# Kernel tuning notes

Hardware: AMD Instinct MI355X
Metric: run time of the kernel (lower is better)

Reference implementation:

```python
import jax, jax.numpy as jnp
import numpy as np

B, C, Hf, T = 8, 2, 257, 2048
D_IN = C * Hf          # 514
DM = 256               # d_model
NL = 4                 # n_layers
N = 32                 # S4D complex state size (d_state=64 -> N=32 complex modes)


def setup_inputs() -> dict:
    key = jax.random.key(0)
    ks = jax.random.split(key, 16)
    sc_in = 1.0 / np.sqrt(D_IN)
    sc_dm = 1.0 / np.sqrt(DM)
    inp = {}
    inp['x'] = jax.random.normal(ks[0], (B, C, Hf, T, 2), dtype=jnp.float32)
    # complex encoder (d_input -> d_model)
    inp['enc_Wr'] = jax.random.normal(ks[1], (DM, D_IN), dtype=jnp.float32) * sc_in
    inp['enc_Wi'] = jax.random.normal(ks[2], (DM, D_IN), dtype=jnp.float32) * sc_in
    inp['enc_br'] = jnp.zeros((DM,), jnp.float32)
    inp['enc_bi'] = jnp.zeros((DM,), jnp.float32)
    # per-layer S4D kernel params (stacked over layers)
    lo, hi = np.log(0.001), np.log(0.1)
    inp['log_dt'] = jax.random.uniform(ks[3], (NL, DM), dtype=jnp.float32) * (hi - lo) + lo
    inp['log_A_real'] = jnp.full((NL, DM, N), np.log(0.5), dtype=jnp.float32)
    inp['A_imag'] = jnp.broadcast_to(np.pi * jnp.arange(N, dtype=jnp.float32), (NL, DM, N)) + 0.0
    inp['C_r'] = jax.random.normal(ks[4], (NL, DM, N), dtype=jnp.float32)
    inp['C_i'] = jax.random.normal(ks[5], (NL, DM, N), dtype=jnp.float32)
    inp['D'] = jax.random.normal(ks[6], (NL, DM), dtype=jnp.float32)
    # per-layer complex pointwise output linear (d_model -> d_model)
    inp['out_Wr'] = jax.random.normal(ks[7], (NL, DM, DM), dtype=jnp.float32) * sc_dm
    inp['out_Wi'] = jax.random.normal(ks[8], (NL, DM, DM), dtype=jnp.float32) * sc_dm
    inp['out_br'] = jnp.zeros((NL, DM), jnp.float32)
    inp['out_bi'] = jnp.zeros((NL, DM), jnp.float32)
    # per-layer complex LayerNorm (separate real/imag affine)
    inp['ln_gamma_r'] = jnp.ones((NL, DM), jnp.float32)
    inp['ln_gamma_i'] = jnp.ones((NL, DM), jnp.float32)
    inp['ln_beta_r'] = jnp.zeros((NL, DM), jnp.float32)
    inp['ln_beta_i'] = jnp.zeros((NL, DM), jnp.float32)
    # complex decoder (d_model -> d_output = c*h)
    inp['dec_Wr'] = jax.random.normal(ks[9], (D_IN, DM), dtype=jnp.float32) * sc_dm
    inp['dec_Wi'] = jax.random.normal(ks[10], (D_IN, DM), dtype=jnp.float32) * sc_dm
    inp['dec_br'] = jnp.zeros((D_IN,), jnp.float32)
    inp['dec_bi'] = jnp.zeros((D_IN,), jnp.float32)
    return inp


def _clinear(xr, xi, Wr, Wi, br, bi):
    # complex linear: (xr + i xi) @ (Wr + i Wi)^T + (br + i bi)
    yr = xr @ Wr.T - xi @ Wi.T + br
    yi = xi @ Wr.T + xr @ Wi.T + bi
    return yr, yi


def _layernorm_ch(v, g, b, eps=1e-5):
    # normalize over channel axis 1 of (B, H, T)
    m = v.mean(axis=1, keepdims=True)
    var = ((v - m) ** 2).mean(axis=1, keepdims=True)
    return (v - m) / jnp.sqrt(var + eps) * g[None, :, None] + b[None, :, None]


def _forward(x, enc_Wr, enc_Wi, enc_br, enc_bi, log_dt, log_A_real, A_imag,
             C_r, C_i, D, out_Wr, out_Wi, out_br, out_bi,
             ln_gamma_r, ln_gamma_i, ln_beta_r, ln_beta_i,
             dec_Wr, dec_Wi, dec_br, dec_bi):
    b, c, h, T, _ = x.shape
    xf = x.reshape(b, c * h, T, 2)
    xf = jnp.swapaxes(xf, 1, 2)               # (b, T, c*h, 2)
    zr, zi = _clinear(xf[..., 0], xf[..., 1], enc_Wr, enc_Wi, enc_br, enc_bi)  # (b, T, DM)
    zr = jnp.swapaxes(zr, -1, -2)             # (b, DM, T)
    zi = jnp.swapaxes(zi, -1, -2)
    tgrid = jnp.arange(T, dtype=jnp.float32)
    n_layers = log_dt.shape[0]
    for l in range(n_layers):
        # ---- ComplexS4D kernel (diagonal SSM, ZOH-like discretization) ----
        dt = jnp.exp(log_dt[l])[:, None]                        # (H,1)
        A = -jnp.exp(log_A_real[l]) + 1j * A_imag[l]            # (H,N) complex
        dtA = A * dt                                            # (H,N)
        Ct = (C_r[l] + 1j * C_i[l]) * (jnp.exp(dtA) - 1.0) / A  # (H,N)
        K = jnp.einsum('hn,hnl->hl', Ct, jnp.exp(dtA[:, :, None] * tgrid))  # complex (H,T)
        # ---- complex FFT causal convolution ----
        u = zr + 1j * zi                                        # (b,H,T)
        y = jnp.fft.ifft(jnp.fft.fft(u, 2 * T) * jnp.fft.fft(K, 2 * T)[None])[..., :T]
        y = y + D[l][None, :, None] * u                         # skip connection
        yr = jax.nn.gelu(y.real)
        yi = jax.nn.gelu(y.imag)
        # ---- complex pointwise output linear ----
        orr = jnp.einsum('bht,gh->bgt', yr, out_Wr[l]) - jnp.einsum('bht,gh->bgt', yi, out_Wi[l]) + out_br[l][None, :, None]
        oii = jnp.einsum('bht,gh->bgt', yi, out_Wr[l]) + jnp.einsum('bht,gh->bgt', yr, out_Wi[l]) + out_bi[l][None, :, None]
        # residual + post-norm (prenorm=False), complex LayerNorm over d_model
        zr = _layernorm_ch(zr + orr, ln_gamma_r[l], ln_beta_r[l])
        zi = _layernorm_ch(zi + oii, ln_gamma_i[l], ln_beta_i[l])
    zr = jnp.swapaxes(zr, -1, -2)             # (b, T, DM)
    zi = jnp.swapaxes(zi, -1, -2)
    dr, di = _clinear(zr, zi, dec_Wr, dec_Wi, dec_br, dec_bi)  # (b, T, c*h)
    dr = jnp.swapaxes(dr, 1, 2)               # (b, c*h, T)
    di = jnp.swapaxes(di, 1, 2)
    return jnp.stack([dr, di], axis=-1).reshape(b, c, h, T, 2)


def reference(x, enc_Wr, enc_Wi, enc_br, enc_bi, log_dt, log_A_real, A_imag,
              C_r, C_i, D, out_Wr, out_Wi, out_br, out_bi,
              ln_gamma_r, ln_gamma_i, ln_beta_r, ln_beta_i,
              dec_Wr, dec_Wi, dec_br, dec_bi):
    return _forward(x, enc_Wr, enc_Wi, enc_br, enc_bi, log_dt, log_A_real, A_imag,
                    C_r, C_i, D, out_Wr, out_Wi, out_br, out_bi,
                    ln_gamma_r, ln_gamma_i, ln_beta_r, ln_beta_i,
                    dec_Wr, dec_Wi, dec_br, dec_bi)
```

## Files before the change

### kernel.cpp

```cpp
#include <hip/hip_runtime.h>
#include <cstddef>
#include <cstdint>


typedef __attribute__((ext_vector_type(8))) short short8;
typedef __attribute__((ext_vector_type(4))) float float4v;

__device__ __forceinline__ unsigned short f2bf(float f) {
    union { float f; unsigned u; } v; v.f = f;
    const unsigned r = v.u + 0x7fffu + ((v.u >> 16) & 1u);
    return (unsigned short)(r >> 16);
}

__device__ __forceinline__ float gelu_tanh(float x) {
    const float x3 = x * x * x;
    const float v  = 0.7978845608028654f * (x + 0.044715f * x3);
    const float e  = __expf(2.f * v);
    const float th = 1.f - 2.f / (e + 1.f);
    return 0.5f * x * (1.f + th);
}

template<int CTL>
__device__ __forceinline__ float dppadd(float x) {
    union { float f; int i; } a, r;
    a.f = x;
    r.i = __builtin_amdgcn_update_dpp(a.i, a.i, CTL, 0xF, 0xF, true);
    return x + r.f;
}
#define DPP_XOR1 0xB1
#define DPP_XOR2 0x4E

#define ASYNC_COPY16(gp, lp) __builtin_amdgcn_global_load_lds( \
    (const __attribute__((address_space(1))) unsigned int*)(gp), \
    (__attribute__((address_space(3))) unsigned int*)(lp), 16, 0, 0)

__global__ __launch_bounds__(256) void buildw_k(
    const float* __restrict__ Wr, const float* __restrict__ Wi,
    unsigned short* __restrict__ A, int G, int H, int Hoff, int Kp, int Mp)
{
    const long long i = (long long)blockIdx.x * 256 + threadIdx.x;
    if (i >= (long long)Mp * Kp) return;
    const int m = (int)(i / Kp), k = (int)(i % Kp);
    float val = 0.f;
    if (m < 2 * G) {
        const int ri = m >= G;
        const int g = m - ri * G;
        const int blk = k >= Hoff;
        const int hh = k - blk * Hoff;
        if (hh < H) {
            const float wr = Wr[(size_t)g * H + hh];
            const float wi = Wi[(size_t)g * H + hh];
            val = ri ? (blk ? wr : wi) : (blk ? -wi : wr);
        }
    }
    A[i] = f2bf(val);
}

__global__ __launch_bounds__(256) void buildwL_k(
    const float* __restrict__ Wr0, const float* __restrict__ Wi0,
    unsigned short* __restrict__ A0)
{
    const int l = blockIdx.y;
    const float* Wr = Wr0 + (size_t)l * 65536;
    const float* Wi = Wi0 + (size_t)l * 65536;
    unsigned short* A = A0 + (size_t)l * 262144;
    const int i = blockIdx.x * 256 + threadIdx.x;
    const int m = i >> 9, k = i & 511;
    const int ri = m >= 256;
    const int g = m & 255;
    const int blk = k >> 8;
    const int hh = k & 255;
    const float wr = Wr[(size_t)g * 256 + hh];
    const float wi = Wi[(size_t)g * 256 + hh];
    const float val = ri ? (blk ? wr : wi) : (blk ? -wi : wr);
    A[i] = f2bf(val);
}

__global__ __launch_bounds__(256) void build_bias_k(
    const float* __restrict__ br, const float* __restrict__ bi,
    float* __restrict__ bias, int G)
{
    const int i = blockIdx.x * 256 + threadIdx.x;
    if (i < G) bias[i] = br[i];
    else if (i < 2 * G) bias[i] = bi[i - G];
}

__global__ __launch_bounds__(256) void build_biasL_k(
    const float* __restrict__ br0, const float* __restrict__ bi0,
    float* __restrict__ bias0)
{
    const int l = blockIdx.y;
    const int i = blockIdx.x * 256 + threadIdx.x;
    const float* br = br0 + l * 256;
    const float* bi = bi0 + l * 256;
    float* bias = bias0 + l * 512;
    if (i < 256) bias[i] = br[i];
    else bias[i] = bi[i - 256];
}

__global__ __launch_bounds__(256) void packx_k(const float* __restrict__ x,
                                               unsigned short* __restrict__ xp)
{
    const int t0 = blockIdx.x * 64, d0 = blockIdx.y * 64, b = blockIdx.z;
    __shared__ unsigned short tr_[64][72];
    __shared__ unsigned short ti_[64][72];
    const int tid = threadIdx.x;
    const int tp = tid & 31, dl0 = tid >> 5;
#pragma unroll
    for (int p = 0; p < 8; ++p) {
        const int d = dl0 + p * 8;
        const int gd = d0 + d;
        float4 v = make_float4(0.f, 0.f, 0.f, 0.f);
        if (gd < 514) v = *(const float4*)(x + (((size_t)b * 514 + gd) * 2048 + t0 + tp * 2) * 2);
        tr_[tp * 2 + 0][d] = f2bf(v.x); ti_[tp * 2 + 0][d] = f2bf(v.y);
        tr_[tp * 2 + 1][d] = f2bf(v.z); ti_[tp * 2 + 1][d] = f2bf(v.w);
    }
    __syncthreads();
    const int dc = tid & 7;
    const int kloc = d0 + dc * 8;
    if (kloc < 528) {
#pragma unroll
        for (int p = 0; p < 2; ++p) {
            const int t = (tid >> 3) + p * 32;
            const size_t rowb = ((size_t)b * 2048 + t0 + t) * 1056;
            *(short8*)&xp[rowb + kloc]       = *(const short8*)&tr_[t][dc * 8];
            *(short8*)&xp[rowb + 528 + kloc] = *(const short8*)&ti_[t][dc * 8];
        }
    }
}

__global__ __launch_bounds__(256) void trz_k(const float* __restrict__ sf,
                                             unsigned short* __restrict__ dst)
{
    const int t0 = blockIdx.x * 64, k0 = blockIdx.y * 64, b = blockIdx.z;
    __shared__ unsigned short tile[64][72];
    const int tid = threadIdx.x;
    const int tp = tid & 31, kl0 = tid >> 5;
#pragma unroll
    for (int p = 0; p < 8; ++p) {
        const int kl = kl0 + p * 8;
        const float2 v = *(const float2*)(sf + ((size_t)b * 512 + k0 + kl) * 2048 + t0 + tp * 2);
        tile[tp * 2 + 0][kl] = f2bf(v.x);
        tile[tp * 2 + 1][kl] = f2bf(v.y);
    }
    __syncthreads();
    const int dc = tid & 7;
#pragma unroll
    for (int p = 0; p < 2; ++p) {
        const int t = (tid >> 3) + p * 32;
        *(short8*)&dst[((size_t)b * 2048 + t0 + t) * 512 + k0 + dc * 8] = *(const short8*)&tile[t][dc * 8];
    }
}

template<int MODE>
__global__ __launch_bounds__(256, 2) void mgemm_k(
    const unsigned short* __restrict__ A, const float* __restrict__ bias,
    const unsigned short* __restrict__ Bm, float* __restrict__ out,
    int M, int Kp)
{
    __shared__ unsigned short As[4096];
    __shared__ unsigned short Bs[4096];
    const int tid = threadIdx.x;
    const int w = tid >> 6, lane = tid & 63;
    const int m0 = blockIdx.x * 128, t0 = blockIdx.y * 128, b = blockIdx.z;
    const int wm = w & 1, wn = w >> 1;

    const unsigned short* Ab = A + (size_t)m0 * Kp;
    const unsigned short* Bb = Bm + ((size_t)b * 2048 + t0) * Kp;

    const int c0 = w * 64 + lane;
    const int r0 = c0 >> 2, q0 = (c0 & 3) * 8;
    const int c1 = c0 + 256;
    const int r1 = c1 >> 2, q1 = (c1 & 3) * 8;
    unsigned short* As0 = &As[(size_t)(w * 64) * 8];
    unsigned short* As1 = &As[(size_t)(w * 64 + 256) * 8];
    unsigned short* Bs0 = &Bs[(size_t)(w * 64) * 8];
    unsigned short* Bs1 = &Bs[(size_t)(w * 64 + 256) * 8];

    float4v acc[4][4];
#pragma unroll
    for (int i = 0; i < 4; ++i)
#pragma unroll
        for (int j = 0; j < 4; ++j) acc[i][j] = (float4v){0.f, 0.f, 0.f, 0.f};

    const int arow = wm * 64 + (lane & 15);
    const int brow = wn * 64 + (lane & 15);
    const int kq = (lane >> 4) * 8;

    for (int k0 = 0; k0 < Kp; k0 += 32) {
        ASYNC_COPY16(Ab + (size_t)r0 * Kp + k0 + q0, As0);
        ASYNC_COPY16(Ab + (size_t)r1 * Kp + k0 + q1, As1);
        ASYNC_COPY16(Bb + (size_t)r0 * Kp + k0 + q0, Bs0);
        ASYNC_COPY16(Bb + (size_t)r1 * Kp + k0 + q1, Bs1);
        __syncthreads();
        short8 af[4], bf[4];
#pragma unroll
        for (int i = 0; i < 4; ++i) af[i] = *(const short8*)&As[(arow + i * 16) * 32 + kq];
#pragma unroll
        for (int j = 0; j < 4; ++j) bf[j] = *(const short8*)&Bs[(brow + j * 16) * 32 + kq];
#pragma unroll
        for (int i = 0; i < 4; ++i)
#pragma unroll
            for (int j = 0; j < 4; ++j)
                acc[i][j] = __builtin_amdgcn_mfma_f32_16x16x32_bf16(af[i], bf[j], acc[i][j], 0, 0, 0);
        __syncthreads();
    }

    const int col = lane & 15;
    const int rq = (lane >> 4) * 4;
#pragma unroll
    for (int i = 0; i < 4; ++i) {
        const int mloc = wm * 64 + i * 16 + rq;
#pragma unroll
        for (int r = 0; r < 4; ++r) {
            const int m = m0 + mloc + r;
            if (MODE == 1 && m >= M) continue;
            const float bs = bias[m];
#pragma unroll
            for (int j = 0; j < 4; ++j) {
                const int t = t0 + wn * 64 + j * 16 + col;
                const float vv = acc[i][j][r] + bs;
                if (MODE == 0) {
                    out[((size_t)b * 512 + m) * 2048 + t] = vv;
                } else {
                    const int comp = m >= 514;
                    const int g = m - 514 * comp;
                    out[(((size_t)b * 514 + g) * 2048 + t) * 2 + comp] = vv;
                }
            }
        }
    }
}

__global__ __launch_bounds__(512, 2) void mgemmln_k(
    const unsigned short* __restrict__ A, const float* __restrict__ bias,
    const unsigned short* __restrict__ Bm, float* __restrict__ z,
    const float* __restrict__ gamr, const float* __restrict__ gami,
    const float* __restrict__ betr, const float* __restrict__ beti, int l)
{
    __shared__ unsigned short Bs[64][512];
    __shared__ float biasS[512], gamS[512], betS[512];
    __shared__ float sred[8][64][2];
    __shared__ float sstat[2][64][2];
    const int tid = threadIdx.x;
    const int w = tid >> 6, lane = tid & 63;
    const int t0g = blockIdx.x * 64, b = blockIdx.y;
    unsigned char* BsB = (unsigned char*)&Bs[0][0];

    {
        const unsigned short* ysrc = Bm + (size_t)b * 512 * 2048 + t0g;
        const int tseg = lane & 7;
        const int rloc = lane >> 3;
#pragma unroll
        for (int p = 0; p < 8; ++p) {
            const int krow = w * 8 + rloc + p * 64;
            const short8 v = *(const short8*)(ysrc + (size_t)krow * 2048 + tseg * 8);
#pragma unroll
            for (int j = 0; j < 8; ++j) {
                const int t = tseg * 8 + j;
                const int mask = (((t & 7) ^ ((t >> 3) & 7)) << 4);
                *(unsigned short*)(BsB + t * 1024 + ((krow * 2) ^ mask)) =
                    ((const unsigned short*)&v)[j];
            }
        }
        const int m = tid, g = m & 255, comp = m >> 8;
        biasS[m] = bias[m];
        gamS[m] = (comp ? gami : gamr)[l * 256 + g];
        betS[m] = (comp ? beti : betr)[l * 256 + g];
    }
    __syncthreads();

    float4v acc[4][4];
#pragma unroll
    for (int i = 0; i < 4; ++i)
#pragma unroll
        for (int j = 0; j < 4; ++j) acc[i][j] = (float4v){0.f, 0.f, 0.f, 0.f};

    const int brow = lane & 15;
    const int kq8 = (lane >> 4) * 8;
    const unsigned short* Ab = A + ((size_t)(w * 64 + brow)) * 512 + kq8;
    int baseB[4], maskB[4];
#pragma unroll
    for (int j = 0; j < 4; ++j) {
        const int t = j * 16 + brow;
        baseB[j] = t * 1024;
        maskB[j] = (((t & 7) ^ ((t >> 3) & 7)) << 4);
    }

#define LOADF(af_, bf_, k0_) do {                                              \
    _Pragma("unroll")                                                          \
    for (int i = 0; i < 4; ++i)                                                \
        af_[i] = *(const short8*)(Ab + (size_t)i * 16 * 512 + (k0_));          \
    _Pragma("unroll")                                                          \
    for (int j = 0; j < 4; ++j)                                                \
        bf_[j] = *(const short8*)(BsB + baseB[j] + ((((k0_) + kq8) * 2) ^ maskB[j])); \
} while (0)
#define MFMAS(af_, bf_) do {                                                   \
    _Pragma("unroll")                                                          \
    for (int i = 0; i < 4; ++i)                                                \
        _Pragma("unroll")                                                      \
        for (int j = 0; j < 4; ++j)                                            \
            acc[i][j] = __builtin_amdgcn_mfma_f32_16x16x32_bf16(af_[i], bf_[j], acc[i][j], 0, 0, 0); \
} while (0)

    {
        short8 afA[4], bfA[4], afB[4], bfB[4];
        LOADF(afA, bfA, 0);
#pragma unroll 1
        for (int kk = 0; kk < 16; kk += 2) {
            LOADF(afB, bfB, kk * 32 + 32);
            MFMAS(afA, bfA);
            if (kk + 2 < 16) LOADF(afA, bfA, kk * 32 + 64);
            MFMAS(afB, bfB);
        }
    }
#undef LOADF
#undef MFMAS

    const int q4 = (lane >> 4) * 4;
    float4 b4[4], g4[4], e4[4];
#pragma unroll
    for (int i = 0; i < 4; ++i) {
        const int m0 = w * 64 + i * 16 + q4;
        b4[i] = *(const float4*)&biasS[m0];
        g4[i] = *(const float4*)&gamS[m0];
        e4[i] = *(const float4*)&betS[m0];
    }

    float s1[4], s2[4];
#pragma unroll
    for (int j = 0; j < 4; ++j) { s1[j] = 0.f; s2[j] = 0.f; }
#pragma unroll
    for (int j = 0; j < 4; ++j) {
        const int t = t0g + j * 16 + brow;
#pragma unroll
        for (int i = 0; i < 4; ++i) {
            const int m = w * 64 + i * 16 + q4;
            const float* zp = &z[((size_t)b * 512 + m) * 2048 + t];
            const float bb[4] = {b4[i].x, b4[i].y, b4[i].z, b4[i].w};
#pragma unroll
            for (int r = 0; r < 4; ++r) {
                const float v = acc[i][j][r] + bb[r] + zp[(size_t)r * 2048];
                acc[i][j][r] = v;
                s1[j] += v; s2[j] += v * v;
            }
        }
    }
#pragma unroll
    for (int j = 0; j < 4; ++j) {
        s1[j] += __shfl_xor(s1[j], 16); s2[j] += __shfl_xor(s2[j], 16);
        s1[j] += __shfl_xor(s1[j], 32); s2[j] += __shfl_xor(s2[j], 32);
    }
    if (lane < 16) {
#pragma unroll
        for (int j = 0; j < 4; ++j) {
            sred[w][j * 16 + lane][0] = s1[j];
            sred[w][j * 16 + lane][1] = s2[j];
        }
    }
    __syncthreads();
    if (tid < 128) {
        const int t = tid & 63, comp = tid >> 6;
        float S1 = 0.f, S2 = 0.f;
#pragma unroll
        for (int w2 = 0; w2 < 4; ++w2) {
            S1 += sred[comp * 4 + w2][t][0];
            S2 += sred[comp * 4 + w2][t][1];
        }
        const float mn = S1 * (1.f / 256.f);
        const float var = S2 * (1.f / 256.f) - mn * mn;
        sstat[comp][t][0] = mn;
        sstat[comp][t][1] = rsqrtf(var + 1e-5f);
    }
    __syncthreads();
    const int comp = w >> 2;
#pragma unroll
    for (int j = 0; j < 4; ++j) {
        const int tl = j * 16 + brow;
        const float mn = sstat[comp][tl][0], rs = sstat[comp][tl][1];
        const int t = t0g + tl;
#pragma unroll
        for (int i = 0; i < 4; ++i) {
            const int m = w * 64 + i * 16 + q4;
            float* zp = &z[((size_t)b * 512 + m) * 2048 + t];
            const float gg[4] = {g4[i].x, g4[i].y, g4[i].z, g4[i].w};
            const float ee[4] = {e4[i].x, e4[i].y, e4[i].z, e4[i].w};
#pragma unroll
            for (int r = 0; r < 4; ++r)
                zp[(size_t)r * 2048] = (acc[i][j][r] - mn) * rs * gg[r] + ee[r];
        }
    }
}

__global__ __launch_bounds__(256, 4) void s4scan_k(
    const float* __restrict__ z, unsigned short* __restrict__ y,
    const float* __restrict__ log_dt, const float* __restrict__ log_A_real,
    const float* __restrict__ A_imag, const float* __restrict__ C_r,
    const float* __restrict__ C_i, const float* __restrict__ Dsk, int l)
{
    const int h = blockIdx.x, b = blockIdx.y;
    const int tid = threadIdx.x;
    const int lane = tid & 63, wv = tid >> 6;
    __shared__ float2 wsh[32], csh[32];
    __shared__ float dsh;
    __shared__ float2 us[64][33];
    __shared__ __align__(16) unsigned char uni[64 * 33 * 8];
    float2 (*vsh2)[33] = (float2(*)[33])uni;
    float2 (*ys)[33]   = (float2(*)[33])uni;

    if (tid < 32) {
        const size_t pidx = ((size_t)l * 256 + h) * 32 + tid;
        const float dt = __expf(log_dt[l * 256 + h]);
        const float Ar = -__expf(log_A_real[pidx]);
        const float Ai = A_imag[pidx];
        const float er = __expf(Ar * dt);
        float sv, cv;
        __sincosf(Ai * dt, &sv, &cv);
        const float wr = er * cv, wi = er * sv;
        const float den = 1.f / (Ar * Ar + Ai * Ai);
        const float nr = wr - 1.f, ni = wi;
        const float qr = (nr * Ar + ni * Ai) * den;
        const float qi = (ni * Ar - nr * Ai) * den;
        const float cr = C_r[pidx], ci = C_i[pidx];
        wsh[tid] = make_float2(wr, wi);
        csh[tid] = make_float2(cr * qr - ci * qi, cr * qi + ci * qr);
    }
    if (tid == 32) dsh = Dsk[l * 256 + h];

    const int c0q = tid >> 2, t0q = (tid & 3) * 8;
    {
        const float* zrp = z + ((size_t)b * 512 + h) * 2048 + tid * 8;
        const float* zip = zrp + 256 * 2048;
        const float4 r0 = *(const float4*)zrp, r1 = *(const float4*)(zrp + 4);
        const float4 i0 = *(const float4*)zip, i1 = *(const float4*)(zip + 4);
        float2* up = &us[c0q][t0q];
        up[0] = make_float2(r0.x, i0.x); up[1] = make_float2(r0.y, i0.y);
        up[2] = make_float2(r0.z, i0.z); up[3] = make_float2(r0.w, i0.w);
        up[4] = make_float2(r1.x, i1.x); up[5] = make_float2(r1.y, i1.y);
        up[6] = make_float2(r1.z, i1.z); up[7] = make_float2(r1.w, i1.w);
    }
    __syncthreads();

    {
        float2 w8[8], x8[8];
#pragma unroll
        for (int j = 0; j < 8; ++j) {
            w8[j] = wsh[wv * 8 + j];
            x8[j] = make_float2(0.f, 0.f);
        }
#pragma unroll 8
        for (int tt = 0; tt < 32; ++tt) {
            const float2 u = us[lane][tt];
#pragma unroll
            for (int j = 0; j < 8; ++j) {
                const float nxr = __builtin_fmaf(w8[j].x, x8[j].x, __builtin_fmaf(-w8[j].y, x8[j].y, u.x));
                const float nxi = __builtin_fmaf(w8[j].x, x8[j].y, __builtin_fmaf(w8[j].y, x8[j].x, u.y));
                x8[j].x = nxr; x8[j].y = nxi;
            }
        }
#pragma unroll
        for (int j = 0; j < 8; ++j) {
            float fr = w8[j].x, fi = w8[j].y;
#pragma unroll
            for (int s = 0; s < 5; ++s) { const float a2 = fr * fr - fi * fi, b2 = 2.f * fr * fi; fr = a2; fi = b2; }
            float qrv = x8[j].x, qiv = x8[j].y, pr = fr, pi = fi;
#pragma unroll
            for (int s = 0; s < 6; ++s) {
                const int d = 1 << s;
                const float sr = __shfl_up(qrv, (unsigned)d);
                const float si = __shfl_up(qiv, (unsigned)d);
                if (lane >= d) {
                    qrv += pr * sr - pi * si;
                    qiv += pr * si + pi * sr;
                }
                const float a2 = pr * pr - pi * pi, b2 = 2.f * pr * pi;
                pr = a2; pi = b2;
            }
            float vr = __shfl_up(qrv, 1u);
            float vi = __shfl_up(qiv, 1u);
            if (lane == 0) { vr = 0.f; vi = 0.f; }
            vsh2[lane][wv * 8 + j] = make_float2(vr, vi);
        }
    }
    __syncthreads();

    {
        const int q = tid & 3;
        float2 w8[8], c8[8], s8[8];
#pragma unroll
        for (int j = 0; j < 8; ++j) {
            const int n = q * 8 + j;
            w8[j] = wsh[n];
            c8[j] = csh[n];
            s8[j] = vsh2[c0q][n];
        }
        __syncthreads();
#pragma unroll 4
        for (int tt = 0; tt < 32; ++tt) {
            const float2 u = us[c0q][tt];
            float pyr = 0.f, pyi = 0.f;
#pragma unroll
            for (int j = 0; j < 8; ++j) {
                const float nsr = __builtin_fmaf(w8[j].x, s8[j].x, __builtin_fmaf(-w8[j].y, s8[j].y, u.x));
                const float nsi = __builtin_fmaf(w8[j].x, s8[j].y, __builtin_fmaf(w8[j].y, s8[j].x, u.y));
                s8[j].x = nsr; s8[j].y = nsi;
                pyr = __builtin_fmaf(c8[j].x, nsr, __builtin_fmaf(-c8[j].y, nsi, pyr));
                pyi = __builtin_fmaf(c8[j].x, nsi, __builtin_fmaf(c8[j].y, nsr, pyi));
            }
            pyr = dppadd<DPP_XOR1>(pyr); pyr = dppadd<DPP_XOR2>(pyr);
            pyi = dppadd<DPP_XOR1>(pyi); pyi = dppadd<DPP_XOR2>(pyi);
            if (q == 0) ys[c0q][tt] = make_float2(pyr, pyi);
        }
    }
    __syncthreads();

    {
        const float dv = dsh;
        unsigned short* yrp = y + ((size_t)b * 512 + h) * 2048 + tid * 8;
        unsigned short* yip = yrp + 256 * 2048;
        short8 vr8, vi8;
#pragma unroll
        for (int j = 0; j < 8; ++j) {
            const float2 yv = ys[c0q][t0q + j];
            const float2 uv = us[c0q][t0q + j];
            ((unsigned short*)&vr8)[j] = f2bf(gelu_tanh(__builtin_fmaf(dv, uv.x, yv.x)));
            ((unsigned short*)&vi8)[j] = f2bf(gelu_tanh(__builtin_fmaf(dv, uv.y, yv.y)));
        }
        *(short8*)yrp = vr8;
        *(short8*)yip = vi8;
    }
}

extern "C" void kernel_launch(void* const* d_in, const int* in_sizes, int n_in,
                              void* d_out, int out_size, void* d_ws, size_t ws_size,
                              hipStream_t stream)
{
    const float* x        = (const float*)d_in[0];
    const float* enc_Wr   = (const float*)d_in[1];
    const float* enc_Wi   = (const float*)d_in[2];
    const float* enc_br   = (const float*)d_in[3];
    const float* enc_bi   = (const float*)d_in[4];
    const float* log_dt   = (const float*)d_in[5];
    const float* log_A_r  = (const float*)d_in[6];
    const float* A_imag   = (const float*)d_in[7];
    const float* C_r      = (const float*)d_in[8];
    const float* C_i      = (const float*)d_in[9];
    const float* Dp       = (const float*)d_in[10];
    const float* out_Wr   = (const float*)d_in[11];
    const float* out_Wi   = (const float*)d_in[12];
    const float* out_br   = (const float*)d_in[13];
    const float* out_bi   = (const float*)d_in[14];
    const float* ln_gr    = (const float*)d_in[15];
    const float* ln_gi    = (const float*)d_in[16];
    const float* ln_br    = (const float*)d_in[17];
    const float* ln_bi    = (const float*)d_in[18];
    const float* dec_Wr   = (const float*)d_in[19];
    const float* dec_Wi   = (const float*)d_in[20];
    const float* dec_br   = (const float*)d_in[21];
    const float* dec_bi   = (const float*)d_in[22];

    uint8_t* W = (uint8_t*)d_ws;
    float* z             = (float*)W;
    unsigned short* zp   = (unsigned short*)(W + 33554432);
    unsigned short* A_enc= (unsigned short*)(W + 50331648);
    unsigned short* A_lay= (unsigned short*)(W + 51412992);
    unsigned short* A_dec= (unsigned short*)(W + 53510144);
    float* b_enc         = (float*)(W + 54689792);
    float* b_lay         = (float*)(W + 54691840);
    float* b_dec         = (float*)(W + 54700032);

    unsigned short* y   = (unsigned short*)((uint8_t*)d_out + 33554432);
    unsigned short* xp  = (unsigned short*)d_out;

    buildw_k<<<2112, 256, 0, stream>>>(enc_Wr, enc_Wi, A_enc, 256, 514, 528, 1056, 512);
    buildwL_k<<<dim3(1024, 4), 256, 0, stream>>>(out_Wr, out_Wi, A_lay);
    buildw_k<<<2304, 256, 0, stream>>>(dec_Wr, dec_Wi, A_dec, 514, 256, 256, 512, 1152);
    build_bias_k<<<2, 256, 0, stream>>>(enc_br, enc_bi, b_enc, 256);
    build_biasL_k<<<dim3(2, 4), 256, 0, stream>>>(out_br, out_bi, b_lay);
    build_bias_k<<<5, 256, 0, stream>>>(dec_br, dec_bi, b_dec, 514);

    packx_k<<<dim3(32, 9, 8), 256, 0, stream>>>(x, xp);
    mgemm_k<0><<<dim3(4, 16, 8), 256, 0, stream>>>(A_enc, b_enc, xp, z, 512, 1056);

    for (int l = 0; l < 4; ++l) {
        s4scan_k<<<dim3(256, 8), 256, 0, stream>>>(z, y, log_dt, log_A_r, A_imag, C_r, C_i, Dp, l);
        mgemmln_k<<<dim3(32, 8), 512, 0, stream>>>(A_lay + (size_t)l * 262144,
                                                   b_lay + l * 512, y, z,
                                                   ln_gr, ln_gi, ln_br, ln_bi, l);
    }

    trz_k<<<dim3(32, 8, 8), 256, 0, stream>>>(z, zp);
    mgemm_k<1><<<dim3(9, 16, 8), 256, 0, stream>>>(A_dec, b_dec, zp, (float*)d_out, 1028, 512);
}
```

Measured before the change: 593.3 us.

## Fuse decoder transpose into GEMM, merge weight-build kernels, trim scan shuffle

The separate z-transpose/bf16-pack kernel and the decoder GEMM are replaced by one decoder kernel. It loads fp32 z directly, converts it to bf16 into a swizzled LDS tile covering the full K=512, and streams A fragments from global memory with double-buffered registers. The six weight and bias preparation launches are merged into a single kernel. The scan replaces a shuffle-up with a shifted LDS store. The aim is to cut launch overhead and the zp round trip through memory, at the cost of redundant z reads across the three M-blocks and uncached global A loads.

```diff
diff --git a/kernel.cpp b/kernel.cpp
--- a/kernel.cpp
+++ b/kernel.cpp
@@ -34,68 +34,85 @@
     (const __attribute__((address_space(1))) unsigned int*)(gp), \
     (__attribute__((address_space(3))) unsigned int*)(lp), 16, 0, 0)
 
-__global__ __launch_bounds__(256) void buildw_k(
-    const float* __restrict__ Wr, const float* __restrict__ Wi,
-    unsigned short* __restrict__ A, int G, int H, int Hoff, int Kp, int Mp)
+__global__ __launch_bounds__(256) void buildall_k(
+    const float* __restrict__ enc_Wr, const float* __restrict__ enc_Wi,
+    const float* __restrict__ out_Wr, const float* __restrict__ out_Wi,
+    const float* __restrict__ dec_Wr, const float* __restrict__ dec_Wi,
+    const float* __restrict__ enc_br, const float* __restrict__ enc_bi,
+    const float* __restrict__ out_br, const float* __restrict__ out_bi,
+    const float* __restrict__ dec_br, const float* __restrict__ dec_bi,
+    unsigned short* __restrict__ A_enc, unsigned short* __restrict__ A_lay,
+    unsigned short* __restrict__ A_dec,
+    float* __restrict__ b_enc, float* __restrict__ b_lay,
+    float* __restrict__ b_dec)
 {
-    const long long i = (long long)blockIdx.x * 256 + threadIdx.x;
-    if (i >= (long long)Mp * Kp) return;
-    const int m = (int)(i / Kp), k = (int)(i % Kp);
-    float val = 0.f;
-    if (m < 2 * G) {
-        const int ri = m >= G;
-        const int g = m - ri * G;
-        const int blk = k >= Hoff;
-        const int hh = k - blk * Hoff;
-        if (hh < H) {
-            const float wr = Wr[(size_t)g * H + hh];
-            const float wi = Wi[(size_t)g * H + hh];
-            val = ri ? (blk ? wr : wi) : (blk ? -wi : wr);
-        }
-    }
-    A[i] = f2bf(val);
-}
-
-__global__ __launch_bounds__(256) void buildwL_k(
-    const float* __restrict__ Wr0, const float* __restrict__ Wi0,
-    unsigned short* __restrict__ A0)
-{
-    const int l = blockIdx.y;
-    const float* Wr = Wr0 + (size_t)l * 65536;
-    const float* Wi = Wi0 + (size_t)l * 65536;
-    unsigned short* A = A0 + (size_t)l * 262144;
-    const int i = blockIdx.x * 256 + threadIdx.x;
-    const int m = i >> 9, k = i & 511;
-    const int ri = m >= 256;
-    const int g = m & 255;
-    const int blk = k >> 8;
-    const int hh = k & 255;
-    const float wr = Wr[(size_t)g * 256 + hh];
-    const float wi = Wi[(size_t)g * 256 + hh];
-    const float val = ri ? (blk ? wr : wi) : (blk ? -wi : wr);
-    A[i] = f2bf(val);
-}
-
-__global__ __launch_bounds__(256) void build_bias_k(
-    const float* __restrict__ br, const float* __restrict__ bi,
-    float* __restrict__ bias, int G)
-{
-    const int i = blockIdx.x * 256 + threadIdx.x;
-    if (i < G) bias[i] = br[i];
-    else if (i < 2 * G) bias[i] = bi[i - G];
-}
-
-__global__ __launch_bounds__(256) void build_biasL_k(
-    const float* __restrict__ br0, const float* __restrict__ bi0,
-    float* __restrict__ bias0)
-{
-    const int l = blockIdx.y;
-    const int i = blockIdx.x * 256 + threadIdx.x;
-    const float* br = br0 + l * 256;
-    const float* bi = bi0 + l * 256;
-    float* bias = bias0 + l * 512;
-    if (i < 256) bias[i] = br[i];
-    else bias[i] = bi[i - 256];
+    int blk = blockIdx.x;
+    const int tid = threadIdx.x;
+    if (blk < 2112) {
+        const int i = blk * 256 + tid;
+        const int m = i / 1056, k = i - m * 1056;
+        const int ri = m >= 256, g = m & 255;
+        const int blk2 = k >= 528;
+        const int hh = k - blk2 * 528;
+        float val = 0.f;
+        if (hh < 514) {
+            const float wr = enc_Wr[(size_t)g * 514 + hh];
+            const float wi = enc_Wi[(size_t)g * 514 + hh];
+            val = ri ? (blk2 ? wr : wi) : (blk2 ? -wi : wr);
+        }
+        A_enc[i] = f2bf(val);
+        return;
+    }
+    blk -= 2112;
+    if (blk < 4096) {
+        const int l = blk >> 10;
+        const int i = ((blk & 1023) << 8) + tid;
+        const float* Wr = out_Wr + (size_t)l * 65536;
+        const float* Wi = out_Wi + (size_t)l * 65536;
+        const int m = i >> 9, k = i & 511;
+        const int ri = m >= 256, g = m & 255;
+        const int blk2 = k >> 8, hh = k & 255;
+        const float wr = Wr[(size_t)g * 256 + hh];
+        const float wi = Wi[(size_t)g * 256 + hh];
+        A_lay[(size_t)l * 262144 + i] =
+            f2bf(ri ? (blk2 ? wr : wi) : (blk2 ? -wi : wr));
+        return;
+    }
+    blk -= 4096;
+    if (blk < 2304) {
+        const int i = blk * 256 + tid;
+        const int m = i >> 9, k = i & 511;
+        float val = 0.f;
+        if (m < 1028) {
+            const int ri = m >= 514;
+            const int g = m - 514 * ri;
+            const int blk2 = k >> 8, hh = k & 255;
+            const float wr = dec_Wr[(size_t)g * 256 + hh];
+            const float wi = dec_Wi[(size_t)g * 256 + hh];
+            val = ri ? (blk2 ? wr : wi) : (blk2 ? -wi : wr);
+        }
+        A_dec[i] = f2bf(val);
+        return;
+    }
+    blk -= 2304;
+    if (blk < 2) {
+        const int i = blk * 256 + tid;
+        b_enc[i] = (i < 256) ? enc_br[i] : enc_bi[i - 256];
+        return;
+    }
+    blk -= 2;
+    if (blk < 8) {
+        const int l = blk >> 1;
+        const int i = ((blk & 1) << 8) + tid;
+        b_lay[l * 512 + i] = (i < 256) ? out_br[l * 256 + i]
+                                       : out_bi[l * 256 + i - 256];
+        return;
+    }
+    blk -= 8;
+    {
+        const int i = blk * 256 + tid;
+        if (i < 1028) b_dec[i] = (i < 514) ? dec_br[i] : dec_bi[i - 514];
+    }
 }
 
 __global__ __launch_bounds__(256) void packx_k(const float* __restrict__ x,
@@ -129,30 +146,6 @@
     }
 }
 
-__global__ __launch_bounds__(256) void trz_k(const float* __restrict__ sf,
-                                             unsigned short* __restrict__ dst)
-{
-    const int t0 = blockIdx.x * 64, k0 = blockIdx.y * 64, b = blockIdx.z;
-    __shared__ unsigned short tile[64][72];
-    const int tid = threadIdx.x;
-    const int tp = tid & 31, kl0 = tid >> 5;
-#pragma unroll
-    for (int p = 0; p < 8; ++p) {
-        const int kl = kl0 + p * 8;
-        const float2 v = *(const float2*)(sf + ((size_t)b * 512 + k0 + kl) * 2048 + t0 + tp * 2);
-        tile[tp * 2 + 0][kl] = f2bf(v.x);
-        tile[tp * 2 + 1][kl] = f2bf(v.y);
-    }
-    __syncthreads();
-    const int dc = tid & 7;
-#pragma unroll
-    for (int p = 0; p < 2; ++p) {
-        const int t = (tid >> 3) + p * 32;
-        *(short8*)&dst[((size_t)b * 2048 + t0 + t) * 512 + k0 + dc * 8] = *(const short8*)&tile[t][dc * 8];
-    }
-}
-
-template<int MODE>
 __global__ __launch_bounds__(256, 2) void mgemm_k(
     const unsigned short* __restrict__ A, const float* __restrict__ bias,
     const unsigned short* __restrict__ Bm, float* __restrict__ out,
@@ -214,19 +207,11 @@
 #pragma unroll
         for (int r = 0; r < 4; ++r) {
             const int m = m0 + mloc + r;
-            if (MODE == 1 && m >= M) continue;
             const float bs = bias[m];
 #pragma unroll
             for (int j = 0; j < 4; ++j) {
                 const int t = t0 + wn * 64 + j * 16 + col;
-                const float vv = acc[i][j][r] + bs;
-                if (MODE == 0) {
-                    out[((size_t)b * 512 + m) * 2048 + t] = vv;
-                } else {
-                    const int comp = m >= 514;
-                    const int g = m - 514 * comp;
-                    out[(((size_t)b * 514 + g) * 2048 + t) * 2 + comp] = vv;
-                }
+                out[((size_t)b * 512 + m) * 2048 + t] = acc[i][j][r] + bs;
             }
         }
     }
@@ -388,6 +373,103 @@
 #pragma unroll
             for (int r = 0; r < 4; ++r)
                 zp[(size_t)r * 2048] = (acc[i][j][r] - mn) * rs * gg[r] + ee[r];
+        }
+    }
+}
+
+__global__ __launch_bounds__(512, 2) void mgemmdec_k(
+    const unsigned short* __restrict__ A, const float* __restrict__ bias,
+    const float* __restrict__ z, float* __restrict__ out)
+{
+    __shared__ unsigned short Bs[64][512];
+    const int tid = threadIdx.x;
+    const int w = tid >> 6, lane = tid & 63;
+    const int m0b = blockIdx.x * 384;
+    const int t0g = blockIdx.y * 64, b = blockIdx.z;
+    unsigned char* BsB = (unsigned char*)&Bs[0][0];
+
+    {
+        const float* zsrc = z + (size_t)b * 512 * 2048 + t0g;
+        const int tseg = lane & 7, rloc = lane >> 3;
+#pragma unroll
+        for (int p = 0; p < 8; ++p) {
+            const int krow = w * 8 + rloc + p * 64;
+            const float* rowp = zsrc + (size_t)krow * 2048 + tseg * 8;
+            const float4 va = *(const float4*)rowp;
+            const float4 vb = *(const float4*)(rowp + 4);
+            const float vals[8] = {va.x, va.y, va.z, va.w, vb.x, vb.y, vb.z, vb.w};
+#pragma unroll
+            for (int j = 0; j < 8; ++j) {
+                const int t = tseg * 8 + j;
+                const int mask = (((t & 7) ^ ((t >> 3) & 7)) << 4);
+                *(unsigned short*)(BsB + t * 1024 + ((krow * 2) ^ mask)) = f2bf(vals[j]);
+            }
+        }
+    }
+    __syncthreads();
+
+    float4v acc[3][4];
+#pragma unroll
+    for (int i = 0; i < 3; ++i)
+#pragma unroll
+        for (int j = 0; j < 4; ++j) acc[i][j] = (float4v){0.f, 0.f, 0.f, 0.f};
+
+    const int brow = lane & 15;
+    const int kq8 = (lane >> 4) * 8;
+    const unsigned short* Ab = A + ((size_t)(m0b + w * 48 + brow)) * 512 + kq8;
+    int baseB[4], maskB[4];
+#pragma unroll
+    for (int j = 0; j < 4; ++j) {
+        const int t = j * 16 + brow;
+        baseB[j] = t * 1024;
+        maskB[j] = (((t & 7) ^ ((t >> 3) & 7)) << 4);
+    }
+
+#define LOADF(af_, bf_, k0_) do {                                              \
+    _Pragma("unroll")                                                          \
+    for (int i = 0; i < 3; ++i)                                                \
+        af_[i] = *(const short8*)(Ab + (size_t)i * 16 * 512 + (k0_));          \
+    _Pragma("unroll")                                                          \
+    for (int j = 0; j < 4; ++j)                                                \
+        bf_[j] = *(const short8*)(BsB + baseB[j] + ((((k0_) + kq8) * 2) ^ maskB[j])); \
+} while (0)
+#define MFMAS(af_, bf_) do {                                                   \
+    _Pragma("unroll")                                                          \
+    for (int i = 0; i < 3; ++i)                                                \
+        _Pragma("unroll")                                                      \
+        for (int j = 0; j < 4; ++j)                                            \
+            acc[i][j] = __builtin_amdgcn_mfma_f32_16x16x32_bf16(af_[i], bf_[j], acc[i][j], 0, 0, 0); \
+} while (0)
+
+    {
+        short8 afA[3], bfA[4], afB[3], bfB[4];
+        LOADF(afA, bfA, 0);
+#pragma unroll 1
+        for (int kk = 0; kk < 16; kk += 2) {
+            LOADF(afB, bfB, kk * 32 + 32);
+            MFMAS(afA, bfA);
+            if (kk + 2 < 16) LOADF(afA, bfA, kk * 32 + 64);
+            MFMAS(afB, bfB);
+        }
+    }
+#undef LOADF
+#undef MFMAS
+
+    const int q4 = (lane >> 4) * 4;
+#pragma unroll
+    for (int i = 0; i < 3; ++i) {
+#pragma unroll
+        for (int r = 0; r < 4; ++r) {
+            const int m = m0b + w * 48 + i * 16 + q4 + r;
+            if (m >= 1028) continue;
+            const float bs = bias[m];
+            const int comp = m >= 514;
+            const int g = m - 514 * comp;
+#pragma unroll
+            for (int j = 0; j < 4; ++j) {
+                const int t = t0g + j * 16 + brow;
+                out[(((size_t)b * 514 + g) * 2048 + t) * 2 + comp] = acc[i][j][r] + bs;
+            }
         }
     }
 }
@@ -458,6 +540,7 @@
                 x8[j].x = nxr; x8[j].y = nxi;
             }
         }
+        const int dstc = (lane + 1) & 63;
 #pragma unroll
         for (int j = 0; j < 8; ++j) {
             float fr = w8[j].x, fi = w8[j].y;
@@ -476,10 +559,8 @@
                 const float a2 = pr * pr - pi * pi, b2 = 2.f * pr * pi;
                 pr = a2; pi = b2;
             }
-            float vr = __shfl_up(qrv, 1u);
-            float vi = __shfl_up(qiv, 1u);
-            if (lane == 0) { vr = 0.f; vi = 0.f; }
-            vsh2[lane][wv * 8 + j] = make_float2(vr, vi);
+            vsh2[dstc][wv * 8 + j] = (lane == 63) ? make_float2(0.f, 0.f)
+                                                  : make_float2(qrv, qiv);
         }
     }
     __syncthreads();
@@ -561,7 +642,6 @@
 
     uint8_t* W = (uint8_t*)d_ws;
     float* z             = (float*)W;
-    unsigned short* zp   = (unsigned short*)(W + 33554432);
     unsigned short* A_enc= (unsigned short*)(W + 50331648);
     unsigned short* A_lay= (unsigned short*)(W + 51412992);
     unsigned short* A_dec= (unsigned short*)(W + 53510144);
@@ -572,15 +652,14 @@
     unsigned short* y   = (unsigned short*)((uint8_t*)d_out + 33554432);
     unsigned short* xp  = (unsigned short*)d_out;
 
-    buildw_k<<<2112, 256, 0, stream>>>(enc_Wr, enc_Wi, A_enc, 256, 514, 528, 1056, 512);
-    buildwL_k<<<dim3(1024, 4), 256, 0, stream>>>(out_Wr, out_Wi, A_lay);
-    buildw_k<<<2304, 256, 0, stream>>>(dec_Wr, dec_Wi, A_dec, 514, 256, 256, 512, 1152);
-    build_bias_k<<<2, 256, 0, stream>>>(enc_br, enc_bi, b_enc, 256);
-    build_biasL_k<<<dim3(2, 4), 256, 0, stream>>>(out_br, out_bi, b_lay);
-    build_bias_k<<<5, 256, 0, stream>>>(dec_br, dec_bi, b_dec, 514);
+    buildall_k<<<8527, 256, 0, stream>>>(enc_Wr, enc_Wi, out_Wr, out_Wi,
+                                         dec_Wr, dec_Wi, enc_br, enc_bi,
+                                         out_br, out_bi, dec_br, dec_bi,
+                                         A_enc, A_lay, A_dec,
+                                         b_enc, b_lay, b_dec);
 
     packx_k<<<dim3(32, 9, 8), 256, 0, stream>>>(x, xp);
-    mgemm_k<0><<<dim3(4, 16, 8), 256, 0, stream>>>(A_enc, b_enc, xp, z, 512, 1056);
+    mgemm_k<<<dim3(4, 16, 8), 256, 0, stream>>>(A_enc, b_enc, xp, z, 512, 1056);
 
     for (int l = 0; l < 4; ++l) {
         s4scan_k<<<dim3(256, 8), 256, 0, stream>>>(z, y, log_dt, log_A_r, A_imag, C_r, C_i, Dp, l);
@@ -589,6 +668,5 @@
                                                    ln_gr, ln_gi, ln_br, ln_bi, l);
     }
 
-    trz_k<<<dim3(32, 8, 8), 256, 0, stream>>>(z, zp);
-    mgemm_k<1><<<dim3(9, 16, 8), 256, 0, stream>>>(A_dec, b_dec, zp, (float*)d_out, 1028, 512);
-}
+    mgemmdec_k<<<dim3(3, 32, 8), 512, 0, stream>>>(A_dec, b_dec, z, (float*)d_out);
+}
```

New measurement: 603.7 us. About the same (+1.7%).
